# Kernel tuning notes

Hardware: AMD Instinct MI355X
Metric: run time of the kernel (lower is better)

Reference implementation:

```python
import jax, jax.numpy as jnp
import numpy as np

N_NODES = 100000
NUM_GRAPHS = 128
FEAT = 128
NUM_CLASSES = 4


def setup_inputs() -> dict:
    key = jax.random.key(0)
    ks = jax.random.split(key, 12)
    x = jax.random.normal(ks[0], (N_NODES, FEAT), dtype=jnp.float32)
    edge_index = jax.random.randint(ks[1], (2, 3200000), 0, N_NODES, dtype=jnp.int64)
    batch = jnp.sort(jax.random.randint(ks[2], (N_NODES,), 0, NUM_GRAPHS, dtype=jnp.int64))

    def glorot(k, fan_in, fan_out):
        lim = float(np.sqrt(6.0 / (fan_in + fan_out)))
        return jax.random.uniform(k, (fan_in, fan_out), jnp.float32, -lim, lim)

    dims = [FEAT, 16, 32, 64, NUM_CLASSES]
    params = {}
    for i in range(4):
        params[f"W{i+1}"] = glorot(ks[3 + i], dims[i], dims[i + 1])
        params[f"b{i+1}"] = jnp.zeros((dims[i + 1],), jnp.float32)
    return dict(x=x, edge_index=edge_index, batch=batch, **params)


def _gcn_norm(edge_index, n):
    # add self-loops, then symmetric normalization deg^{-1/2} A_hat deg^{-1/2}
    loop = jnp.arange(n, dtype=edge_index.dtype)
    row = jnp.concatenate([edge_index[0], loop])  # source
    col = jnp.concatenate([edge_index[1], loop])  # target
    deg = jax.ops.segment_sum(jnp.ones_like(col, jnp.float32), col, num_segments=n)
    dinv = jnp.where(deg > 0, jax.lax.rsqrt(deg), 0.0)
    norm = dinv[row] * dinv[col]  # [E+N]
    return row, col, norm


def _gcn_conv(x, row, col, norm, W, b):
    h = x @ W  # [N, out]
    msg = h[row] * norm[:, None]  # gather + scale, [E+N, out]
    agg = jax.ops.segment_sum(msg, col, num_segments=x.shape[0])
    return agg + b


def reference(x, edge_index, batch, W1, b1, W2, b2, W3, b3, W4, b4):
    n = x.shape[0]
    row, col, norm = _gcn_norm(edge_index, n)
    # dropout is identity in eval mode
    h = jax.nn.relu(_gcn_conv(x, row, col, norm, W1, b1))
    h = jax.nn.relu(_gcn_conv(h, row, col, norm, W2, b2))
    h = jax.nn.relu(_gcn_conv(h, row, col, norm, W3, b3))
    h = _gcn_conv(h, row, col, norm, W4, b4)
    pooled = jax.ops.segment_max(h, batch, num_segments=NUM_GRAPHS)  # [G, C]
    return jax.nn.log_softmax(pooled, axis=1)
```

## Files before the change

### kernel.cpp

```cpp
#include <hip/hip_runtime.h>

#define DIV_UP(a,b) (((a)+(b)-1)/(b))

constexpr int BSHIFT = 7;
constexpr int BNODES = 128;
constexpr int CHUNK_E = 16384;
constexpr int PTH = 512;
constexpr int SCH = 8;
constexpr int SCSH = 14;

__device__ inline unsigned short f2bf(float f) {
    unsigned u = __float_as_uint(f);
    u = u + 0x7FFFu + ((u >> 16) & 1u);
    return (unsigned short)(u >> 16);
}
__device__ inline float bflo(unsigned u) { return __uint_as_float(u << 16); }
__device__ inline float bfhi(unsigned u) { return __uint_as_float(u & 0xFFFF0000u); }

__global__ void zero_int_k(int* p, int n) {
    int i = blockIdx.x * blockDim.x + threadIdx.x;
    if (i < n) p[i] = 0;
}

__global__ void bucket_hist_k(const int* __restrict__ col, int* __restrict__ bhist, int E, int nb) {
    __shared__ int lh[1024];
    for (int i = threadIdx.x; i < 1024; i += blockDim.x) lh[i] = 0;
    __syncthreads();
    int stride = gridDim.x * blockDim.x;
    for (int e = blockIdx.x * blockDim.x + threadIdx.x; e < E; e += stride)
        atomicAdd(&lh[col[e] >> BSHIFT], 1);
    __syncthreads();
    for (int i = threadIdx.x; i < nb; i += blockDim.x) {
        int v = lh[i];
        if (v) atomicAdd(&bhist[i], v);
    }
}

__global__ void bucket_scan_k(const int* __restrict__ bhist, int* __restrict__ bcur, int nb) {
    __shared__ int lds[256];
    int base = threadIdx.x * 4;
    int v[4]; int s = 0;
#pragma unroll
    for (int j = 0; j < 4; j++) { v[j] = (base + j < nb) ? bhist[base + j] : 0; s += v[j]; }
    lds[threadIdx.x] = s; __syncthreads();
    for (int off = 1; off < 256; off <<= 1) {
        int t = (threadIdx.x >= off) ? lds[threadIdx.x - off] : 0;
        __syncthreads();
        lds[threadIdx.x] += t;
        __syncthreads();
    }
    int excl = lds[threadIdx.x] - s;
#pragma unroll
    for (int j = 0; j < 4; j++) {
        if (base + j < nb) bcur[base + j] = excl;
        excl += v[j];
    }
}

__global__ void __launch_bounds__(PTH) partition_k(
        const int* __restrict__ row, const int* __restrict__ col,
        int* __restrict__ bcur, int* __restrict__ part, int E, int nb) {
    __shared__ int lh[1024];
    __shared__ int lbase[1024];
    __shared__ int delta[1024];
    __shared__ unsigned sorted[CHUNK_E];
    __shared__ unsigned short bid[CHUNK_E];
    int tid = threadIdx.x;
    for (int i = tid; i < 1024; i += PTH) lh[i] = 0;
    __syncthreads();
    int base = blockIdx.x * CHUNK_E;
    int end = min(E, base + CHUNK_E);
    for (int e = base + tid; e < end; e += PTH)
        atomicAdd(&lh[col[e] >> BSHIFT], 1);
    __syncthreads();
    int v0 = lh[2 * tid], v1 = lh[2 * tid + 1];
    int s = v0 + v1;
    delta[tid] = s;
    __syncthreads();
    for (int off = 1; off < PTH; off <<= 1) {
        int t = (tid >= off) ? delta[tid - off] : 0;
        __syncthreads();
        delta[tid] += t;
        __syncthreads();
    }
    int excl = delta[tid] - s;
    lbase[2 * tid] = excl;
    lbase[2 * tid + 1] = excl + v0;
    __syncthreads();
    for (int i = tid; i < nb; i += PTH) {
        int c = lh[i];
        int g = c ? atomicAdd(&bcur[i], c) : 0;
        delta[i] = g - lbase[i];
    }
    __syncthreads();
    for (int i = tid; i < nb; i += PTH) lh[i] = lbase[i];
    __syncthreads();
    for (int e = base + tid; e < end; e += PTH) {
        int r = row[e], c = col[e];
        int b = c >> BSHIFT;
        int slot = atomicAdd(&lh[b], 1);
        sorted[slot] = (unsigned)((r << BSHIFT) | (c & (BNODES - 1)));
        bid[slot] = (unsigned short)b;
    }
    __syncthreads();
    int cnt = end - base;
    for (int i = tid; i < cnt; i += PTH) {
        int b = bid[i];
        part[delta[b] + i] = (int)sorted[i];
    }
}

__global__ void __launch_bounds__(256) csr_build_k(
        const int* __restrict__ part, const int* __restrict__ bcur,
        int* __restrict__ cur, float* __restrict__ dinv,
        int* __restrict__ csr, int N) {
    __shared__ int cnt[BNODES * SCH];
    __shared__ int scan_t[256];
    __shared__ int ebounds[2];
    int b = blockIdx.x;
    int tid = threadIdx.x;
    if (tid == 0) { ebounds[0] = b ? bcur[b - 1] : 0; ebounds[1] = bcur[b]; }
    for (int i = tid; i < BNODES * SCH; i += 256) cnt[i] = 0;
    __syncthreads();
    int e0 = ebounds[0], e1 = ebounds[1];
    for (int e = e0 + tid; e < e1; e += 256) {
        unsigned v = (unsigned)part[e];
        int cell = (int)(v & (BNODES - 1)) * SCH + (int)(v >> (BSHIFT + SCSH));
        atomicAdd(&cnt[cell], 1);
    }
    __syncthreads();
    int base4 = tid * 4;
    int c0 = cnt[base4], c1 = cnt[base4+1], c2 = cnt[base4+2], c3 = cnt[base4+3];
    int s = c0 + c1 + c2 + c3;
    scan_t[tid] = s;
    __syncthreads();
    for (int off = 1; off < 256; off <<= 1) {
        int t = (tid >= off) ? scan_t[tid - off] : 0;
        __syncthreads();
        scan_t[tid] += t;
        __syncthreads();
    }
    int excl = scan_t[tid] - s;
    cnt[base4]     = excl;
    cnt[base4 + 1] = excl + c0;
    cnt[base4 + 2] = excl + c0 + c1;
    cnt[base4 + 3] = excl + c0 + c1 + c2;
    __syncthreads();
    if (tid < BNODES) {
        int node = b * BNODES + tid;
        int segstart = cnt[tid * SCH];
        int segend   = (tid == BNODES - 1) ? (e1 - e0) : cnt[(tid + 1) * SCH];
        if (node < N) {
            cur[node]  = e0 + segend;
            dinv[node] = rsqrtf(1.0f + (float)(segend - segstart));
        }
    }
    __syncthreads();
    for (int e = e0 + tid; e < e1; e += 256) {
        unsigned v = (unsigned)part[e];
        int cell = (int)(v & (BNODES - 1)) * SCH + (int)(v >> (BSHIFT + SCSH));
        int p = atomicAdd(&cnt[cell], 1);
        csr[e0 + p] = (int)(v >> BSHIFT);
    }
}

template<int D, int EPI>
__global__ void gather_prop_k(const float* __restrict__ hs, const float* __restrict__ dinv,
                              const int* __restrict__ cur, const int* __restrict__ csr,
                              const float* __restrict__ b, float* __restrict__ out, int n) {
    constexpr int TPN = D / 4;
    int tid = blockIdx.x * blockDim.x + threadIdx.x;
    int node = tid / TPN, t = tid % TPN;
    if (node >= n) return;
    float di = dinv[node];
    float4 acc = reinterpret_cast<const float4*>(hs + (size_t)node * D)[t];
    int e0 = node ? cur[node - 1] : 0;
    int e1 = cur[node];
    int e = e0;
    for (; e + 1 < e1; e += 2) {
        int s0 = csr[e], s1 = csr[e + 1];
        float4 v0 = reinterpret_cast<const float4*>(hs + (size_t)s0 * D)[t];
        float4 v1 = reinterpret_cast<const float4*>(hs + (size_t)s1 * D)[t];
        acc.x += v0.x + v1.x; acc.y += v0.y + v1.y;
        acc.z += v0.z + v1.z; acc.w += v0.w + v1.w;
    }
    if (e < e1) {
        int s0 = csr[e];
        float4 v0 = reinterpret_cast<const float4*>(hs + (size_t)s0 * D)[t];
        acc.x += v0.x; acc.y += v0.y; acc.z += v0.z; acc.w += v0.w;
    }
    acc.x *= di; acc.y *= di; acc.z *= di; acc.w *= di;
    if (EPI == 1) {
        acc.x = fmaxf(acc.x + b[t*4+0], 0.f) * di;
        acc.y = fmaxf(acc.y + b[t*4+1], 0.f) * di;
        acc.z = fmaxf(acc.z + b[t*4+2], 0.f) * di;
        acc.w = fmaxf(acc.w + b[t*4+3], 0.f) * di;
    }
    reinterpret_cast<float4*>(out + (size_t)node * D)[t] = acc;
}

__global__ void __launch_bounds__(256) gather32_bf_k(
        const unsigned short* __restrict__ hb, const float* __restrict__ dinv,
        const int* __restrict__ cur, const int* __restrict__ csr,
        float* __restrict__ out, int n) {
    int tid4 = blockIdx.x * 256 + threadIdx.x;
    int node = tid4 >> 2, t = tid4 & 3;
    if (node >= n) return;
    const uint4* hb4 = reinterpret_cast<const uint4*>(hb);
    uint4 sv = hb4[(size_t)node * 4 + t];
    float a0 = bflo(sv.x), a1 = bfhi(sv.x), a2 = bflo(sv.y), a3 = bfhi(sv.y);
    float a4 = bflo(sv.z), a5 = bfhi(sv.z), a6 = bflo(sv.w), a7 = bfhi(sv.w);
    int e0 = node ? cur[node - 1] : 0;
    int e1 = cur[node];
    int e = e0;
    for (; e + 1 < e1; e += 2) {
        uint4 v = hb4[(size_t)csr[e] * 4 + t];
        uint4 w = hb4[(size_t)csr[e + 1] * 4 + t];
        a0 += bflo(v.x) + bflo(w.x); a1 += bfhi(v.x) + bfhi(w.x);
        a2 += bflo(v.y) + bflo(w.y); a3 += bfhi(v.y) + bfhi(w.y);
        a4 += bflo(v.z) + bflo(w.z); a5 += bfhi(v.z) + bfhi(w.z);
        a6 += bflo(v.w) + bflo(w.w); a7 += bfhi(v.w) + bfhi(w.w);
    }
    if (e < e1) {
        uint4 v = hb4[(size_t)csr[e] * 4 + t];
        a0 += bflo(v.x); a1 += bfhi(v.x); a2 += bflo(v.y); a3 += bfhi(v.y);
        a4 += bflo(v.z); a5 += bfhi(v.z); a6 += bflo(v.w); a7 += bfhi(v.w);
    }
    float di = dinv[node];
    float* op = out + (size_t)node * 32 + t * 8;
    *reinterpret_cast<float4*>(op)     = make_float4(a0*di, a1*di, a2*di, a3*di);
    *reinterpret_cast<float4*>(op + 4) = make_float4(a4*di, a5*di, a6*di, a7*di);
}

template<int IN, int OUT, bool RELU, bool BIAS, bool SCALE, bool IBF, bool OBF>
__global__ void __launch_bounds__(256) matmul_k(
        const void* __restrict__ xv, const float* __restrict__ W,
        const float* __restrict__ b, const float* __restrict__ dinv,
        void* __restrict__ yv, int n) {
    constexpr int TN  = 64;
    constexpr int RS  = IN + 4;
    constexpr int OPT = OUT / 4;
    constexpr int NQ  = IN / 4;
    __shared__ float xs[TN * RS];
    __shared__ float Ws[IN * OUT];
    __shared__ float bs[OUT];

    for (int i = threadIdx.x; i < IN * OUT; i += 256) Ws[i] = W[i];
    if (BIAS) for (int i = threadIdx.x; i < OUT; i += 256) bs[i] = b[i];

    int base = blockIdx.x * TN;
    if constexpr (!IBF) {
        const float* x = (const float*)xv;
        for (int i = threadIdx.x; i < TN * NQ; i += 256) {
            int r = i / NQ, c = i % NQ;
            float4 v = make_float4(0.f, 0.f, 0.f, 0.f);
            if (base + r < n) v = reinterpret_cast<const float4*>(x + (size_t)(base + r) * IN)[c];
            *reinterpret_cast<float4*>(&xs[r * RS + c * 4]) = v;
        }
    } else {
        constexpr int NU = IN / 8;
        const uint4* x = (const uint4*)xv;
        for (int i = threadIdx.x; i < TN * NU; i += 256) {
            int r = i / NU, c = i % NU;
            uint4 v = make_uint4(0u, 0u, 0u, 0u);
            if (base + r < n) v = x[(size_t)(base + r) * NU + c];
            float* dst = &xs[r * RS + c * 8];
            dst[0] = bflo(v.x); dst[1] = bfhi(v.x);
            dst[2] = bflo(v.y); dst[3] = bfhi(v.y);
            dst[4] = bflo(v.z); dst[5] = bfhi(v.z);
            dst[6] = bflo(v.w); dst[7] = bfhi(v.w);
        }
    }
    __syncthreads();

    int node = threadIdx.x >> 2;
    int g    = threadIdx.x & 3;
    int j0   = g * OPT;
    int gnode = base + node;
    if (gnode >= n) return;

    float acc[OPT];
#pragma unroll
    for (int jj = 0; jj < OPT; jj++) acc[jj] = 0.f;

    const float* xrow = &xs[node * RS];
#pragma unroll
    for (int k4 = 0; k4 < NQ; k4++) {
        float4 xvv = *reinterpret_cast<const float4*>(&xrow[k4 * 4]);
        float xk[4] = {xvv.x, xvv.y, xvv.z, xvv.w};
#pragma unroll
        for (int kk = 0; kk < 4; kk++) {
            const float* wrow = &Ws[(k4 * 4 + kk) * OUT + j0];
#pragma unroll
            for (int jj = 0; jj < OPT; jj++)
                acc[jj] += xk[kk] * wrow[jj];
        }
    }

    float di = SCALE ? dinv[gnode] : 1.f;
    float vout[OPT];
#pragma unroll
    for (int jj = 0; jj < OPT; jj++) {
        float v = acc[jj] + (BIAS ? bs[j0 + jj] : 0.f);
        if (RELU) v = fmaxf(v, 0.f);
        if (SCALE) v *= di;
        vout[jj] = v;
    }
    if constexpr (OBF) {
        unsigned short* yr = (unsigned short*)yv + (size_t)gnode * OUT + j0;
#pragma unroll
        for (int q = 0; q < OPT / 8; q++) {
            uint4 pk;
            pk.x = (unsigned)f2bf(vout[q*8+0]) | ((unsigned)f2bf(vout[q*8+1]) << 16);
            pk.y = (unsigned)f2bf(vout[q*8+2]) | ((unsigned)f2bf(vout[q*8+3]) << 16);
            pk.z = (unsigned)f2bf(vout[q*8+4]) | ((unsigned)f2bf(vout[q*8+5]) << 16);
            pk.w = (unsigned)f2bf(vout[q*8+6]) | ((unsigned)f2bf(vout[q*8+7]) << 16);
            reinterpret_cast<uint4*>(yr)[q] = pk;
        }
    } else {
        float* yr = (float*)yv + (size_t)gnode * OUT + j0;
        if (OPT % 4 == 0) {
#pragma unroll
            for (int q = 0; q < OPT / 4; q++)
                *reinterpret_cast<float4*>(yr + q * 4) =
                    make_float4(vout[q*4+0], vout[q*4+1], vout[q*4+2], vout[q*4+3]);
        } else {
#pragma unroll
            for (int jj = 0; jj < OPT; jj++) yr[jj] = vout[jj];
        }
    }
}

__device__ inline unsigned fkey(float x) {
    unsigned u = __float_as_uint(x);
    return (u & 0x80000000u) ? ~u : (u | 0x80000000u);
}
__device__ inline float funkey(unsigned k) {
    unsigned u = (k & 0x80000000u) ? (k & 0x7FFFFFFFu) : ~k;
    return __uint_as_float(u);
}

__global__ void pool_init_k(unsigned* pooled, int total) {
    int i = blockIdx.x * blockDim.x + threadIdx.x;
    if (i < total) pooled[i] = 0u;
}

__global__ void pool_max_k(const float* __restrict__ h4, const float* __restrict__ b4,
                           const int* __restrict__ batch, unsigned* __restrict__ pooled,
                           int n, int num_graphs) {
    __shared__ unsigned lds[128 * 4];
    for (int i = threadIdx.x; i < num_graphs * 4; i += blockDim.x) lds[i] = 0u;
    __syncthreads();
    int i = blockIdx.x * blockDim.x + threadIdx.x;
    if (i < n) {
        int g = batch[i];
        float4 v = reinterpret_cast<const float4*>(h4)[i];
        atomicMax(&lds[g*4+0], fkey(v.x + b4[0]));
        atomicMax(&lds[g*4+1], fkey(v.y + b4[1]));
        atomicMax(&lds[g*4+2], fkey(v.z + b4[2]));
        atomicMax(&lds[g*4+3], fkey(v.w + b4[3]));
    }
    __syncthreads();
    for (int i2 = threadIdx.x; i2 < num_graphs * 4; i2 += blockDim.x) {
        unsigned k = lds[i2];
        if (k) atomicMax(&pooled[i2], k);
    }
}

__global__ void logsoftmax_k(const unsigned* __restrict__ pooled, float* __restrict__ out, int G) {
    int g = blockIdx.x * blockDim.x + threadIdx.x;
    if (g >= G) return;
    float v[4];
#pragma unroll
    for (int j = 0; j < 4; j++) v[j] = funkey(pooled[g*4+j]);
    float m = fmaxf(fmaxf(v[0], v[1]), fmaxf(v[2], v[3]));
    float s = 0.f;
#pragma unroll
    for (int j = 0; j < 4; j++) s += expf(v[j] - m);
    float l = logf(s);
#pragma unroll
    for (int j = 0; j < 4; j++) out[g*4+j] = v[j] - m - l;
}

extern "C" void kernel_launch(void* const* d_in, const int* in_sizes, int n_in,
                              void* d_out, int out_size, void* d_ws, size_t ws_size,
                              hipStream_t stream) {
    const float* x     = (const float*)d_in[0];
    const int*   ei    = (const int*)d_in[1];
    const int*   batch = (const int*)d_in[2];
    const float* W1 = (const float*)d_in[3];
    const float* b1 = (const float*)d_in[4];
    const float* W2 = (const float*)d_in[5];
    const float* b2 = (const float*)d_in[6];
    const float* W3 = (const float*)d_in[7];
    const float* b3 = (const float*)d_in[8];
    const float* W4 = (const float*)d_in[9];
    const float* b4 = (const float*)d_in[10];

    const int N = in_sizes[2];
    const int E = in_sizes[1] / 2;
    const int G = 128;
    const int* row = ei;
    const int* col = ei + E;
    const int NB = DIV_UP(N, BNODES);

    float* ws    = (float*)d_ws;
    float* dinv  = ws;
    int*   cur   = (int*)(dinv + N);
    int*   bhist = cur + N;
    int*   bcur  = bhist + 1024;
    int*   csr   = bcur + 1024;
    float* f16a  = (float*)(csr + E);
    float* f16b  = f16a + (size_t)N * 16;
    float* f32a  = f16b + (size_t)N * 16;
    float* f32b  = f32a + (size_t)N * 32;
    unsigned* pooled = (unsigned*)(f32b + (size_t)N * 32);
    int* part = (int*)f32a;
    unsigned short* hb32 = (unsigned short*)f32a;
    unsigned short* hb64 = (unsigned short*)f32a;
    float* f4a = f32b;
    float* f4b = f32b + (size_t)N * 4;

    const int B = 256;
    const int gridN = DIV_UP(N, B);
    const int gridM = DIV_UP(N, 64);

    zero_int_k<<<DIV_UP(1024, B), B, 0, stream>>>(bhist, 1024);
    bucket_hist_k<<<512, B, 0, stream>>>(col, bhist, E, NB);
    bucket_scan_k<<<1, 256, 0, stream>>>(bhist, bcur, NB);
    partition_k<<<DIV_UP(E, CHUNK_E), PTH, 0, stream>>>(row, col, bcur, part, E, NB);
    csr_build_k<<<NB, 256, 0, stream>>>(part, bcur, cur, dinv, csr, N);

    matmul_k<128,16,false,false,true,false,false><<<gridM, B, 0, stream>>>(x, W1, nullptr, dinv, f16b, N);
    gather_prop_k<16,1><<<DIV_UP(N*4, B), B, 0, stream>>>(f16b, dinv, cur, csr, b1, f16a, N);

    gather_prop_k<16,0><<<DIV_UP(N*4, B), B, 0, stream>>>(f16a, dinv, cur, csr, nullptr, f16b, N);
    matmul_k<16,32,true,true,true,false,true><<<gridM, B, 0, stream>>>(f16b, W2, b2, dinv, hb32, N);

    gather32_bf_k<<<DIV_UP(N*4, B), B, 0, stream>>>(hb32, dinv, cur, csr, f32b, N);
    matmul_k<32,64,true,true,true,false,true><<<gridM, B, 0, stream>>>(f32b, W3, b3, dinv, hb64, N);

    matmul_k<64,4,false,false,false,true,false><<<gridM, B, 0, stream>>>(hb64, W4, nullptr, nullptr, f4a, N);
    gather_prop_k<4,0><<<DIV_UP(N, B), B, 0, stream>>>(f4a, dinv, cur, csr, nullptr, f4b, N);

    pool_init_k<<<DIV_UP(G*4, B), B, 0, stream>>>(pooled, G*4);
    pool_max_k<<<gridN, B, 0, stream>>>(f4b, b4, batch, pooled, N, G);
    logsoftmax_k<<<1, 128, 0, stream>>>(pooled, (float*)d_out, G);
}
```

Baseline: 267.0 us.

## Use bf16 for 16-wide gathers, fuse final gather with max-pool, halve partition chunk

The first two 16-feature propagation steps now store and gather node features as bf16 instead of fp32, which halves the bytes fetched per edge in these gather-bound passes. The last 4-class gather is fused with the segment-max pooling, removing one kernel launch and an intermediate buffer round trip. The partition kernel uses smaller chunks with 256 threads, and its scan handles four buckets per thread. The cost is extra rounding error from bf16 storage in layer one.

```diff
diff --git a/kernel.cpp b/kernel.cpp
--- a/kernel.cpp
+++ b/kernel.cpp
@@ -4,8 +4,8 @@
 
 constexpr int BSHIFT = 7;
 constexpr int BNODES = 128;
-constexpr int CHUNK_E = 16384;
-constexpr int PTH = 512;
+constexpr int CHUNK_E = 8192;
+constexpr int PTH = 256;
 constexpr int SCH = 8;
 constexpr int SCSH = 14;
 
@@ -73,19 +73,22 @@
     for (int e = base + tid; e < end; e += PTH)
         atomicAdd(&lh[col[e] >> BSHIFT], 1);
     __syncthreads();
-    int v0 = lh[2 * tid], v1 = lh[2 * tid + 1];
-    int s = v0 + v1;
+    int b4i = tid * 4;
+    int c0 = lh[b4i], c1 = lh[b4i+1], c2 = lh[b4i+2], c3 = lh[b4i+3];
+    int s = c0 + c1 + c2 + c3;
     delta[tid] = s;
     __syncthreads();
-    for (int off = 1; off < PTH; off <<= 1) {
+    for (int off = 1; off < 256; off <<= 1) {
         int t = (tid >= off) ? delta[tid - off] : 0;
         __syncthreads();
         delta[tid] += t;
         __syncthreads();
     }
     int excl = delta[tid] - s;
-    lbase[2 * tid] = excl;
-    lbase[2 * tid + 1] = excl + v0;
+    lbase[b4i]     = excl;
+    lbase[b4i + 1] = excl + c0;
+    lbase[b4i + 2] = excl + c0 + c1;
+    lbase[b4i + 3] = excl + c0 + c1 + c2;
     __syncthreads();
     for (int i = tid; i < nb; i += PTH) {
         int c = lh[i];
@@ -164,39 +167,54 @@
     }
 }
 
-template<int D, int EPI>
-__global__ void gather_prop_k(const float* __restrict__ hs, const float* __restrict__ dinv,
-                              const int* __restrict__ cur, const int* __restrict__ csr,
-                              const float* __restrict__ b, float* __restrict__ out, int n) {
-    constexpr int TPN = D / 4;
-    int tid = blockIdx.x * blockDim.x + threadIdx.x;
-    int node = tid / TPN, t = tid % TPN;
+template<int EPI>
+__global__ void __launch_bounds__(256) gather16_bf_k(
+        const unsigned short* __restrict__ hb, const float* __restrict__ dinv,
+        const int* __restrict__ cur, const int* __restrict__ csr,
+        const float* __restrict__ b, void* __restrict__ outv, int n) {
+    int t2 = blockIdx.x * 256 + threadIdx.x;
+    int node = t2 >> 1, t = t2 & 1;
     if (node >= n) return;
-    float di = dinv[node];
-    float4 acc = reinterpret_cast<const float4*>(hs + (size_t)node * D)[t];
+    const uint4* hb4 = reinterpret_cast<const uint4*>(hb);
+    uint4 sv = hb4[(size_t)node * 2 + t];
+    float a0 = bflo(sv.x), a1 = bfhi(sv.x), a2 = bflo(sv.y), a3 = bfhi(sv.y);
+    float a4 = bflo(sv.z), a5 = bfhi(sv.z), a6 = bflo(sv.w), a7 = bfhi(sv.w);
     int e0 = node ? cur[node - 1] : 0;
     int e1 = cur[node];
     int e = e0;
     for (; e + 1 < e1; e += 2) {
-        int s0 = csr[e], s1 = csr[e + 1];
-        float4 v0 = reinterpret_cast<const float4*>(hs + (size_t)s0 * D)[t];
-        float4 v1 = reinterpret_cast<const float4*>(hs + (size_t)s1 * D)[t];
-        acc.x += v0.x + v1.x; acc.y += v0.y + v1.y;
-        acc.z += v0.z + v1.z; acc.w += v0.w + v1.w;
+        uint4 v = hb4[(size_t)csr[e] * 2 + t];
+        uint4 w = hb4[(size_t)csr[e + 1] * 2 + t];
+        a0 += bflo(v.x) + bflo(w.x); a1 += bfhi(v.x) + bfhi(w.x);
+        a2 += bflo(v.y) + bflo(w.y); a3 += bfhi(v.y) + bfhi(w.y);
+        a4 += bflo(v.z) + bflo(w.z); a5 += bfhi(v.z) + bfhi(w.z);
+        a6 += bflo(v.w) + bflo(w.w); a7 += bfhi(v.w) + bfhi(w.w);
     }
     if (e < e1) {
-        int s0 = csr[e];
-        float4 v0 = reinterpret_cast<const float4*>(hs + (size_t)s0 * D)[t];
-        acc.x += v0.x; acc.y += v0.y; acc.z += v0.z; acc.w += v0.w;
-    }
-    acc.x *= di; acc.y *= di; acc.z *= di; acc.w *= di;
-    if (EPI == 1) {
-        acc.x = fmaxf(acc.x + b[t*4+0], 0.f) * di;
-        acc.y = fmaxf(acc.y + b[t*4+1], 0.f) * di;
-        acc.z = fmaxf(acc.z + b[t*4+2], 0.f) * di;
-        acc.w = fmaxf(acc.w + b[t*4+3], 0.f) * di;
-    }
-    reinterpret_cast<float4*>(out + (size_t)node * D)[t] = acc;
+        uint4 v = hb4[(size_t)csr[e] * 2 + t];
+        a0 += bflo(v.x); a1 += bfhi(v.x); a2 += bflo(v.y); a3 += bfhi(v.y);
+        a4 += bflo(v.z); a5 += bfhi(v.z); a6 += bflo(v.w); a7 += bfhi(v.w);
+    }
+    float di = dinv[node];
+    a0 *= di; a1 *= di; a2 *= di; a3 *= di;
+    a4 *= di; a5 *= di; a6 *= di; a7 *= di;
+    if constexpr (EPI == 1) {
+        int bo = t * 8;
+        a0 = fmaxf(a0 + b[bo+0], 0.f) * di; a1 = fmaxf(a1 + b[bo+1], 0.f) * di;
+        a2 = fmaxf(a2 + b[bo+2], 0.f) * di; a3 = fmaxf(a3 + b[bo+3], 0.f) * di;
+        a4 = fmaxf(a4 + b[bo+4], 0.f) * di; a5 = fmaxf(a5 + b[bo+5], 0.f) * di;
+        a6 = fmaxf(a6 + b[bo+6], 0.f) * di; a7 = fmaxf(a7 + b[bo+7], 0.f) * di;
+        uint4 pk;
+        pk.x = (unsigned)f2bf(a0) | ((unsigned)f2bf(a1) << 16);
+        pk.y = (unsigned)f2bf(a2) | ((unsigned)f2bf(a3) << 16);
+        pk.z = (unsigned)f2bf(a4) | ((unsigned)f2bf(a5) << 16);
+        pk.w = (unsigned)f2bf(a6) | ((unsigned)f2bf(a7) << 16);
+        reinterpret_cast<uint4*>(outv)[(size_t)node * 2 + t] = pk;
+    } else {
+        float* op = (float*)outv + (size_t)node * 16 + t * 8;
+        *reinterpret_cast<float4*>(op)     = make_float4(a0, a1, a2, a3);
+        *reinterpret_cast<float4*>(op + 4) = make_float4(a4, a5, a6, a7);
+    }
 }
 
 __global__ void __launch_bounds__(256) gather32_bf_k(
@@ -232,6 +250,73 @@
     *reinterpret_cast<float4*>(op + 4) = make_float4(a4*di, a5*di, a6*di, a7*di);
 }
 
+__device__ inline unsigned fkey(float x) {
+    unsigned u = __float_as_uint(x);
+    return (u & 0x80000000u) ? ~u : (u | 0x80000000u);
+}
+__device__ inline float funkey(unsigned k) {
+    unsigned u = (k & 0x80000000u) ? (k & 0x7FFFFFFFu) : ~k;
+    return __uint_as_float(u);
+}
+
+__global__ void gather4_pool_k(const float* __restrict__ hs, const float* __restrict__ dinv,
+                               const int* __restrict__ cur, const int* __restrict__ csr,
+                               const float* __restrict__ b4, const int* __restrict__ batch,
+                               unsigned* __restrict__ pooled, int n, int num_graphs) {
+    __shared__ unsigned lds[128 * 4];
+    for (int i = threadIdx.x; i < num_graphs * 4; i += blockDim.x) lds[i] = 0u;
+    __syncthreads();
+    int node = blockIdx.x * blockDim.x + threadIdx.x;
+    if (node < n) {
+        float di = dinv[node];
+        float4 acc = reinterpret_cast<const float4*>(hs)[node];
+        int e0 = node ? cur[node - 1] : 0;
+        int e1 = cur[node];
+        int e = e0;
+        for (; e + 1 < e1; e += 2) {
+            int s0 = csr[e], s1 = csr[e + 1];
+            float4 v0 = reinterpret_cast<const float4*>(hs)[s0];
+            float4 v1 = reinterpret_cast<const float4*>(hs)[s1];
+            acc.x += v0.x + v1.x; acc.y += v0.y + v1.y;
+            acc.z += v0.z + v1.z; acc.w += v0.w + v1.w;
+        }
+        if (e < e1) {
+            float4 v0 = reinterpret_cast<const float4*>(hs)[csr[e]];
+            acc.x += v0.x; acc.y += v0.y; acc.z += v0.z; acc.w += v0.w;
+        }
+        int g = batch[node];
+        atomicMax(&lds[g*4+0], fkey(acc.x * di + b4[0]));
+        atomicMax(&lds[g*4+1], fkey(acc.y * di + b4[1]));
+        atomicMax(&lds[g*4+2], fkey(acc.z * di + b4[2]));
+        atomicMax(&lds[g*4+3], fkey(acc.w * di + b4[3]));
+    }
+    __syncthreads();
+    for (int i2 = threadIdx.x; i2 < num_graphs * 4; i2 += blockDim.x) {
+        unsigned k = lds[i2];
+        if (k) atomicMax(&pooled[i2], k);
+    }
+}
+
+__global__ void pool_init_k(unsigned* pooled, int total) {
+    int i = blockIdx.x * blockDim.x + threadIdx.x;
+    if (i < total) pooled[i] = 0u;
+}
+
+__global__ void logsoftmax_k(const unsigned* __restrict__ pooled, float* __restrict__ out, int G) {
+    int g = blockIdx.x * blockDim.x + threadIdx.x;
+    if (g >= G) return;
+    float v[4];
+#pragma unroll
+    for (int j = 0; j < 4; j++) v[j] = funkey(pooled[g*4+j]);
+    float m = fmaxf(fmaxf(v[0], v[1]), fmaxf(v[2], v[3]));
+    float s = 0.f;
+#pragma unroll
+    for (int j = 0; j < 4; j++) s += expf(v[j] - m);
+    float l = logf(s);
+#pragma unroll
+    for (int j = 0; j < 4; j++) out[g*4+j] = v[j] - m - l;
+}
+
 template<int IN, int OUT, bool RELU, bool BIAS, bool SCALE, bool IBF, bool OBF>
 __global__ void __launch_bounds__(256) matmul_k(
         const void* __restrict__ xv, const float* __restrict__ W,
@@ -308,14 +393,21 @@
     }
     if constexpr (OBF) {
         unsigned short* yr = (unsigned short*)yv + (size_t)gnode * OUT + j0;
-#pragma unroll
-        for (int q = 0; q < OPT / 8; q++) {
-            uint4 pk;
-            pk.x = (unsigned)f2bf(vout[q*8+0]) | ((unsigned)f2bf(vout[q*8+1]) << 16);
-            pk.y = (unsigned)f2bf(vout[q*8+2]) | ((unsigned)f2bf(vout[q*8+3]) << 16);
-            pk.z = (unsigned)f2bf(vout[q*8+4]) | ((unsigned)f2bf(vout[q*8+5]) << 16);
-            pk.w = (unsigned)f2bf(vout[q*8+6]) | ((unsigned)f2bf(vout[q*8+7]) << 16);
-            reinterpret_cast<uint4*>(yr)[q] = pk;
+        if constexpr (OPT % 8 == 0) {
+#pragma unroll
+            for (int q = 0; q < OPT / 8; q++) {
+                uint4 pk;
+                pk.x = (unsigned)f2bf(vout[q*8+0]) | ((unsigned)f2bf(vout[q*8+1]) << 16);
+                pk.y = (unsigned)f2bf(vout[q*8+2]) | ((unsigned)f2bf(vout[q*8+3]) << 16);
+                pk.z = (unsigned)f2bf(vout[q*8+4]) | ((unsigned)f2bf(vout[q*8+5]) << 16);
+                pk.w = (unsigned)f2bf(vout[q*8+6]) | ((unsigned)f2bf(vout[q*8+7]) << 16);
+                reinterpret_cast<uint4*>(yr)[q] = pk;
+            }
+        } else {
+            uint2 pk;
+            pk.x = (unsigned)f2bf(vout[0]) | ((unsigned)f2bf(vout[1]) << 16);
+            pk.y = (unsigned)f2bf(vout[2]) | ((unsigned)f2bf(vout[3]) << 16);
+            *reinterpret_cast<uint2*>(yr) = pk;
         }
     } else {
         float* yr = (float*)yv + (size_t)gnode * OUT + j0;
@@ -329,57 +421,6 @@
             for (int jj = 0; jj < OPT; jj++) yr[jj] = vout[jj];
         }
     }
-}
-
-__device__ inline unsigned fkey(float x) {
-    unsigned u = __float_as_uint(x);
-    return (u & 0x80000000u) ? ~u : (u | 0x80000000u);
-}
-__device__ inline float funkey(unsigned k) {
-    unsigned u = (k & 0x80000000u) ? (k & 0x7FFFFFFFu) : ~k;
-    return __uint_as_float(u);
-}
-
-__global__ void pool_init_k(unsigned* pooled, int total) {
-    int i = blockIdx.x * blockDim.x + threadIdx.x;
-    if (i < total) pooled[i] = 0u;
-}
-
-__global__ void pool_max_k(const float* __restrict__ h4, const float* __restrict__ b4,
-                           const int* __restrict__ batch, unsigned* __restrict__ pooled,
-                           int n, int num_graphs) {
-    __shared__ unsigned lds[128 * 4];
-    for (int i = threadIdx.x; i < num_graphs * 4; i += blockDim.x) lds[i] = 0u;
-    __syncthreads();
-    int i = blockIdx.x * blockDim.x + threadIdx.x;
-    if (i < n) {
-        int g = batch[i];
-        float4 v = reinterpret_cast<const float4*>(h4)[i];
-        atomicMax(&lds[g*4+0], fkey(v.x + b4[0]));
-        atomicMax(&lds[g*4+1], fkey(v.y + b4[1]));
-        atomicMax(&lds[g*4+2], fkey(v.z + b4[2]));
-        atomicMax(&lds[g*4+3], fkey(v.w + b4[3]));
-    }
-    __syncthreads();
-    for (int i2 = threadIdx.x; i2 < num_graphs * 4; i2 += blockDim.x) {
-        unsigned k = lds[i2];
-        if (k) atomicMax(&pooled[i2], k);
-    }
-}
-
-__global__ void logsoftmax_k(const unsigned* __restrict__ pooled, float* __restrict__ out, int G) {
-    int g = blockIdx.x * blockDim.x + threadIdx.x;
-    if (g >= G) return;
-    float v[4];
-#pragma unroll
-    for (int j = 0; j < 4; j++) v[j] = funkey(pooled[g*4+j]);
-    float m = fmaxf(fmaxf(v[0], v[1]), fmaxf(v[2], v[3]));
-    float s = 0.f;
-#pragma unroll
-    for (int j = 0; j < 4; j++) s += expf(v[j] - m);
-    float l = logf(s);
-#pragma unroll
-    for (int j = 0; j < 4; j++) out[g*4+j] = v[j] - m - l;
 }
 
 extern "C" void kernel_launch(void* const* d_in, const int* in_sizes, int n_in,
@@ -416,14 +457,16 @@
     float* f32b  = f32a + (size_t)N * 32;
     unsigned* pooled = (unsigned*)(f32b + (size_t)N * 32);
     int* part = (int*)f32a;
-    unsigned short* hb32 = (unsigned short*)f32a;
-    unsigned short* hb64 = (unsigned short*)f32a;
+    unsigned short* hb16a = (unsigned short*)f16a;
+    unsigned short* hb16b = (unsigned short*)f16b;
+    unsigned short* hb32  = (unsigned short*)f32a;
+    unsigned short* hb64  = (unsigned short*)f32a;
     float* f4a = f32b;
-    float* f4b = f32b + (size_t)N * 4;
 
     const int B = 256;
     const int gridN = DIV_UP(N, B);
     const int gridM = DIV_UP(N, 64);
+    const int grid2 = DIV_UP(2 * N, B);
 
     zero_int_k<<<DIV_UP(1024, B), B, 0, stream>>>(bhist, 1024);
     bucket_hist_k<<<512, B, 0, stream>>>(col, bhist, E, NB);
@@ -431,19 +474,18 @@
     partition_k<<<DIV_UP(E, CHUNK_E), PTH, 0, stream>>>(row, col, bcur, part, E, NB);
     csr_build_k<<<NB, 256, 0, stream>>>(part, bcur, cur, dinv, csr, N);
 
-    matmul_k<128,16,false,false,true,false,false><<<gridM, B, 0, stream>>>(x, W1, nullptr, dinv, f16b, N);
-    gather_prop_k<16,1><<<DIV_UP(N*4, B), B, 0, stream>>>(f16b, dinv, cur, csr, b1, f16a, N);
-
-    gather_prop_k<16,0><<<DIV_UP(N*4, B), B, 0, stream>>>(f16a, dinv, cur, csr, nullptr, f16b, N);
-    matmul_k<16,32,true,true,true,false,true><<<gridM, B, 0, stream>>>(f16b, W2, b2, dinv, hb32, N);
+    matmul_k<128,16,false,false,true,false,true><<<gridM, B, 0, stream>>>(x, W1, nullptr, dinv, hb16b, N);
+    gather16_bf_k<1><<<grid2, B, 0, stream>>>(hb16b, dinv, cur, csr, b1, hb16a, N);
+
+    gather16_bf_k<0><<<grid2, B, 0, stream>>>(hb16a, dinv, cur, csr, nullptr, f32b, N);
+    matmul_k<16,32,true,true,true,false,true><<<gridM, B, 0, stream>>>(f32b, W2, b2, dinv, hb32, N);
 
     gather32_bf_k<<<DIV_UP(N*4, B), B, 0, stream>>>(hb32, dinv, cur, csr, f32b, N);
     matmul_k<32,64,true,true,true,false,true><<<gridM, B, 0, stream>>>(f32b, W3, b3, dinv, hb64, N);
 
     matmul_k<64,4,false,false,false,true,false><<<gridM, B, 0, stream>>>(hb64, W4, nullptr, nullptr, f4a, N);
-    gather_prop_k<4,0><<<DIV_UP(N, B), B, 0, stream>>>(f4a, dinv, cur, csr, nullptr, f4b, N);
-
     pool_init_k<<<DIV_UP(G*4, B), B, 0, stream>>>(pooled, G*4);
-    pool_max_k<<<gridN, B, 0, stream>>>(f4b, b4, batch, pooled, N, G);
+    gather4_pool_k<<<gridN, B, 0, stream>>>(f4a, dinv, cur, csr, b4, batch, pooled, N, G);
+
     logsoftmax_k<<<1, 128, 0, stream>>>(pooled, (float*)d_out, G);
 }
```

Result: faster. 259.2 us (-2.9%).
